# Performance work log

Hardware: AMD Instinct MI355X
Metric: run time of the kernel (lower is better)

The kernel has to match this reference:

```python
import jax, jax.numpy as jnp
import numpy as np

B, N, C, H = 2, 2048, 768, 12
D = C // H
EPS = 1e-5


def setup_inputs() -> dict:
    key = jax.random.key(0)
    ks = jax.random.split(key, 12)
    s = 0.02
    return {
        "x": jax.random.normal(ks[0], (B, N, C), jnp.float32),
        "attn_mask": jax.random.randint(ks[1], (N, N), 0, 2) > 0,  # True = NOT allowed
        "ln1_g": jnp.ones((C,), jnp.float32),
        "ln1_b": jnp.zeros((C,), jnp.float32),
        "w_qkv": jax.random.normal(ks[2], (C, 3 * C), jnp.float32) * s,  # [in,out]
        "b_qkv": jnp.zeros((3 * C,), jnp.float32),
        "w_proj": jax.random.normal(ks[3], (C, C), jnp.float32) * s,
        "b_proj": jnp.zeros((C,), jnp.float32),
        "ls1": jnp.full((C,), 1e-5, jnp.float32),
        "ln2_g": jnp.ones((C,), jnp.float32),
        "ln2_b": jnp.zeros((C,), jnp.float32),
        "w1": jax.random.normal(ks[4], (C, 4 * C), jnp.float32) * s,
        "b1": jnp.zeros((4 * C,), jnp.float32),
        "w2": jax.random.normal(ks[5], (4 * C, C), jnp.float32) * s,
        "b2": jnp.zeros((C,), jnp.float32),
        "ls2": jnp.full((C,), 1e-5, jnp.float32),
    }


def layer_norm(x, g, b):
    mu = jnp.mean(x, axis=-1, keepdims=True)
    var = jnp.var(x, axis=-1, keepdims=True)
    return (x - mu) * jax.lax.rsqrt(var + EPS) * g + b


def reference(x, attn_mask, ln1_g, ln1_b, w_qkv, b_qkv, w_proj, b_proj, ls1,
              ln2_g, ln2_b, w1, b1, w2, b2, ls2):
    # ---- attention branch ----
    h = layer_norm(x, ln1_g, ln1_b)
    qkv = h @ w_qkv + b_qkv                       # [B,N,3C]
    qkv = qkv.reshape(B, N, 3, H, D).transpose(2, 0, 3, 1, 4)  # [3,B,H,N,D]
    q, k, v = qkv[0], qkv[1], qkv[2]
    scores = jnp.einsum('bhnd,bhmd->bhnm', q, k) * (D ** -0.5)  # [B,H,N,N]
    neg = jnp.finfo(scores.dtype).min
    scores = jnp.where(attn_mask, neg, scores)    # mask broadcasts over B,H
    attn = jax.nn.softmax(scores, axis=-1)
    o = jnp.einsum('bhnm,bhmd->bhnd', attn, v).transpose(0, 2, 1, 3).reshape(B, N, C)
    x = x + (o @ w_proj + b_proj) * ls1
    # ---- MLP branch ----
    h = layer_norm(x, ln2_g, ln2_b)
    h = jax.nn.gelu(h @ w1 + b1, approximate=False)
    x = x + (h @ w2 + b2) * ls2
    return x
```

## Files before the change

### kernel.cpp

```cpp
#include <hip/hip_runtime.h>
#include <hip/hip_bf16.h>
#include <math.h>

#define BN 2
#define SEQ 2048
#define CH 768
#define NH 12
#define HD 64
#define TOK (BN*SEQ)


using bf16_t = __hip_bfloat16;
typedef __attribute__((ext_vector_type(8))) short short8;
typedef __attribute__((ext_vector_type(8))) unsigned short ushort8;
typedef __attribute__((ext_vector_type(4))) float floatx4;
typedef __attribute__((ext_vector_type(2))) unsigned uintx2;

#define OFF_LN1G 0
#define OFF_LN1B 768
#define OFF_BQKV 1536
#define OFF_BPROJ 3840
#define OFF_LS1 4608
#define OFF_LN2G 5376
#define OFF_LN2B 6144
#define OFF_B1 6912
#define OFF_B2 9984
#define OFF_LS2 10752

__device__ inline float b2f(bf16_t v){ return __bfloat162float(v); }
__device__ inline bf16_t f2b(float v){ return __float2bfloat16(v); }
__device__ inline short f2bs(float v){ bf16_t b = __float2bfloat16(v); return *reinterpret_cast<short*>(&b); }
__device__ inline unsigned pk2(float a, float b){
  return (unsigned)(unsigned short)f2bs(a) | ((unsigned)(unsigned short)f2bs(b) << 16);
}
__device__ inline float sane(float v){ return (fabsf(v) < 1e30f) ? v : 0.0f; }
__device__ inline float clampf(float v, float lim){
  v = sane(v);
  return fminf(fmaxf(v, -lim), lim);
}
__device__ inline float ldf(const bf16_t* p){ return __bfloat162float(*p); }
__device__ inline float ldf(const float* p){ return *p; }
__device__ inline bool bf16_mode(const void* gref){
  return *reinterpret_cast<const unsigned*>(gref) == 0x3F803F80u;
}
__device__ inline void gload16(const void* g, void* l){
  __builtin_amdgcn_global_load_lds(
      (const __attribute__((address_space(1))) unsigned int*)g,
      (__attribute__((address_space(3))) unsigned int*)l, 16, 0, 0);
}

template<typename T>
__device__ inline void tr32(const T* __restrict__ src, size_t colOff, int stride,
    bf16_t* __restrict__ dst, int dstStride, int r0, int c0, float* smem, int tid)
{
  const int tx = tid & 31, ty = tid >> 5;
  #pragma unroll
  for (int j = 0; j < 4; j++)
    smem[(ty + j*8)*33 + tx] = ldf(src + (size_t)(r0 + ty + j*8) * stride + colOff + c0 + tx);
  __syncthreads();
  #pragma unroll
  for (int j = 0; j < 4; j++)
    dst[(size_t)(c0 + ty + j*8) * dstStride + r0 + tx] = f2b(smem[tx*33 + ty + j*8]);
}

template<typename T, bool GUARDED>
__global__ __launch_bounds__(256) void prep1_kernel(
    const T* __restrict__ x, const T* __restrict__ w_qkv, const T* __restrict__ w_proj,
    const T* __restrict__ w1, const T* __restrict__ w2,
    const T* __restrict__ g1, const T* __restrict__ b1_, const T* __restrict__ bqkv,
    const T* __restrict__ bproj, const T* __restrict__ ls1, const T* __restrict__ g2,
    const T* __restrict__ b2_, const T* __restrict__ bb1, const T* __restrict__ bb2,
    const T* __restrict__ ls2, const void* __restrict__ mask,
    float* __restrict__ pb, bf16_t* __restrict__ wqkvT, bf16_t* __restrict__ wprojT,
    unsigned long long* __restrict__ m1, bf16_t* __restrict__ a1,
    bf16_t* __restrict__ w1T, bf16_t* __restrict__ w2T,
    const void* __restrict__ gref)
{
  if (GUARDED && (bf16_mode(gref) != (sizeof(T) == 2))) return;
  __shared__ float smem[1056];
  const int tid = threadIdx.x;
  int wg = blockIdx.x;

  if (wg < 4096) {
    const T* xr = x + (size_t)wg * CH;
    float v0 = sane(ldf(xr + tid)), v1 = sane(ldf(xr + tid + 256)), v2 = sane(ldf(xr + tid + 512));
    float s  = v0 + v1 + v2;
    float s2 = v0*v0 + v1*v1 + v2*v2;
    #pragma unroll
    for (int o = 32; o > 0; o >>= 1) { s += __shfl_down(s, o, 64); s2 += __shfl_down(s2, o, 64); }
    if ((tid & 63) == 0) { smem[tid >> 6] = s; smem[(tid >> 6) + 4] = s2; }
    __syncthreads();
    if (tid == 0) {
      float ts = smem[0] + smem[1] + smem[2] + smem[3];
      float tq = smem[4] + smem[5] + smem[6] + smem[7];
      float mu = ts * (1.f / CH);
      float var = tq * (1.f / CH) - mu * mu;
      smem[8] = mu; smem[9] = rsqrtf(fmaxf(var, 0.f) + 1e-5f);
    }
    __syncthreads();
    const float mu = smem[8], rs = smem[9];
    bf16_t* orow = a1 + (size_t)wg * CH;
    orow[tid      ] = f2b(clampf((v0 - mu) * rs * ldf(g1 + tid      ) + ldf(b1_ + tid      ), 32.f));
    orow[tid + 256] = f2b(clampf((v1 - mu) * rs * ldf(g1 + tid + 256) + ldf(b1_ + tid + 256), 32.f));
    orow[tid + 512] = f2b(clampf((v2 - mu) * rs * ldf(g1 + tid + 512) + ldf(b1_ + tid + 512), 32.f));
    return;
  }
  wg -= 4096;
  if (wg < 1728) {
    tr32(w_qkv, 0, 2304, wqkvT, 768, (wg / 72) * 32, (wg % 72) * 32, smem, tid);
    return;
  }
  wg -= 1728;
  if (wg < 576) {
    tr32(w_proj, 0, 768, wprojT, 768, (wg / 24) * 32, (wg % 24) * 32, smem, tid);
    return;
  }
  wg -= 576;
  if (wg < 512) {
    const unsigned* mw = (const unsigned*)mask;
    unsigned accu = 0;
    #pragma unroll 8
    for (int i = 0; i < 64; i++) accu |= mw[i];
    const bool is8 = (accu > 1u);
    const int wave = tid >> 6, lane = tid & 63;
    #pragma unroll 4
    for (int i = 0; i < 32; i++) {
      const int word = wg * 128 + wave * 32 + i;
      const size_t elem = (size_t)word * 64 + lane;
      bool pred;
      if (is8) pred = ((const unsigned char*)mask)[elem] != 0;
      else     pred = ((const int*)mask)[elem] != 0;
      unsigned long long bits = __ballot(pred);
      if (lane == 0) m1[word] = bits;
    }
    return;
  }
  wg -= 512;
  if (wg < 1) {
    #define PCOPY(off, src, n) for (int i = tid; i < (n); i += 256) pb[(off)+i] = ldf((src)+i);
    PCOPY(OFF_LN1G, g1, 768)
    PCOPY(OFF_LN1B, b1_, 768)
    PCOPY(OFF_BQKV, bqkv, 2304)
    PCOPY(OFF_BPROJ, bproj, 768)
    PCOPY(OFF_LS1, ls1, 768)
    PCOPY(OFF_LN2G, g2, 768)
    PCOPY(OFF_LN2B, b2_, 768)
    PCOPY(OFF_B1, bb1, 3072)
    PCOPY(OFF_B2, bb2, 768)
    PCOPY(OFF_LS2, ls2, 768)
    #undef PCOPY
    return;
  }
  wg -= 1;
  if (wg < 2304) {
    tr32(w1, 0, 3072, w1T, 768, (wg / 96) * 32, (wg % 96) * 32, smem, tid);
    return;
  }
  wg -= 2304;
  {
    tr32(w2, 0, 768, w2T, 3072, (wg / 24) * 32, (wg % 24) * 32, smem, tid);
    return;
  }
}

template<typename T, bool GUARDED>
__global__ __launch_bounds__(256) void trc_kernel(const T* __restrict__ w1,
    const T* __restrict__ w2, bf16_t* __restrict__ w1Tc, bf16_t* __restrict__ w2Tc,
    int kc, const void* __restrict__ gref)
{
  if (GUARDED && (bf16_mode(gref) != (sizeof(T) == 2))) return;
  __shared__ float smem[1056];
  const int tid = threadIdx.x;
  int wg = blockIdx.x;
  if (wg < 576) {
    tr32(w1, (size_t)kc * 768, 3072, w1Tc, 768, (wg / 24) * 32, (wg % 24) * 32, smem, tid);
  } else {
    wg -= 576;
    tr32(w2 + (size_t)kc * 768 * 768, 0, 768, w2Tc, 768, (wg / 24) * 32, (wg % 24) * 32, smem, tid);
  }
}

__global__ __launch_bounds__(256) void ln2x_kernel(const bf16_t* __restrict__ x1,
    bf16_t* __restrict__ a2, const float* __restrict__ pb)
{
  __shared__ float red[10];
  const int row = blockIdx.x, tid = threadIdx.x;
  const bf16_t* xr = x1 + (size_t)row * CH;
  float v0 = sane(ldf(xr + tid)), v1 = sane(ldf(xr + tid + 256)), v2 = sane(ldf(xr + tid + 512));
  float s  = v0 + v1 + v2;
  float s2 = v0*v0 + v1*v1 + v2*v2;
  #pragma unroll
  for (int o = 32; o > 0; o >>= 1) { s += __shfl_down(s, o, 64); s2 += __shfl_down(s2, o, 64); }
  if ((tid & 63) == 0) { red[tid >> 6] = s; red[(tid >> 6) + 4] = s2; }
  __syncthreads();
  if (tid == 0) {
    float ts = red[0] + red[1] + red[2] + red[3];
    float tq = red[4] + red[5] + red[6] + red[7];
    float mu = ts * (1.f / CH);
    float var = tq * (1.f / CH) - mu * mu;
    red[8] = mu; red[9] = rsqrtf(fmaxf(var, 0.f) + 1e-5f);
  }
  __syncthreads();
  const float mu = red[8], rs = red[9];
  bf16_t* orow = a2 + (size_t)row * CH;
  orow[tid      ] = f2b(clampf((v0 - mu) * rs * pb[OFF_LN2G + tid      ] + pb[OFF_LN2B + tid      ], 32.f));
  orow[tid + 256] = f2b(clampf((v1 - mu) * rs * pb[OFF_LN2G + tid + 256] + pb[OFF_LN2B + tid + 256], 32.f));
  orow[tid + 512] = f2b(clampf((v2 - mu) * rs * pb[OFF_LN2G + tid + 512] + pb[OFF_LN2B + tid + 512], 32.f));
}

template<int MODE, int MT, int NT>
__global__ __launch_bounds__(256) void mgemm(
    const bf16_t* __restrict__ A, const bf16_t* __restrict__ BT,
    const float* __restrict__ pb, const int K, const int ldb,
    const int biasOff, const int scaleOff,
    const void* __restrict__ resid, const void* __restrict__ gref,
    bf16_t* __restrict__ o0, bf16_t* __restrict__ o1, bf16_t* __restrict__ vtout,
    float* __restrict__ oF, const bf16_t* __restrict__ stg,
    const int addPrev, const int finalize)
{
  constexpr int MI = MT / 32;
  constexpr int NI = NT / 32;
  __shared__ __align__(16) short As[MT * 32];
  __shared__ __align__(16) short Bs[NT * 32];
  const int tid = threadIdx.x;
  const int wave = tid >> 6, lane = tid & 63, lane15 = lane & 15, quad = lane >> 4;
  const int wr = (wave >> 1) * (MT / 2), wc = (wave & 1) * (NT / 2);
  const int mBase = blockIdx.y * MT;
  const int nBase = blockIdx.x * NT;

  floatx4 acc[MI][NI];
  #pragma unroll
  for (int mi = 0; mi < MI; mi++)
    #pragma unroll
    for (int ni = 0; ni < NI; ni++) acc[mi][ni] = (floatx4){0.f, 0.f, 0.f, 0.f};

  const bf16_t* aS0 = A  + (size_t)(mBase + (tid >> 2)) * K + (tid & 3) * 8;
  const bf16_t* aS1 = aS0 + (size_t)64 * K;
  const bf16_t* bS0 = BT + (size_t)(nBase + (tid >> 2)) * ldb + (tid & 3) * 8;
  const bf16_t* bS1 = bS0 + (size_t)64 * ldb;
  const int wfl = __builtin_amdgcn_readfirstlane(wave);
  short* aD0 = &As[wfl * 512];
  short* aD1 = (MT == 128) ? &As[2048 + wfl * 512] : nullptr;
  short* bD0 = &Bs[wfl * 512];
  short* bD1 = (NT == 128) ? &Bs[2048 + wfl * 512] : nullptr;

  for (int k0 = 0; k0 < K; k0 += 32) {
    __syncthreads();
    gload16(aS0 + k0, aD0);
    if (MT == 128) gload16(aS1 + k0, aD1);
    gload16(bS0 + k0, bD0);
    if (NT == 128) gload16(bS1 + k0, bD1);
    __syncthreads();
    short8 av[MI], bv[NI];
    #pragma unroll
    for (int mi = 0; mi < MI; mi++)
      av[mi] = *(const short8*)&As[(wr + mi * 16 + lane15) * 32 + quad * 8];
    #pragma unroll
    for (int ni = 0; ni < NI; ni++)
      bv[ni] = *(const short8*)&Bs[(wc + ni * 16 + lane15) * 32 + quad * 8];
    #pragma unroll
    for (int mi = 0; mi < MI; mi++)
      #pragma unroll
      for (int ni = 0; ni < NI; ni++)
        acc[mi][ni] = __builtin_amdgcn_mfma_f32_16x16x32_bf16(av[mi], bv[ni], acc[mi][ni], 0, 0, 0);
  }

  const bool rbf = (MODE == 1) ? bf16_mode(gref) : false;
  #pragma unroll
  for (int mi = 0; mi < MI; mi++) {
    #pragma unroll
    for (int ni = 0; ni < NI; ni++) {
      const int c0u = nBase + wc + ni * 16;
      const int col = c0u + lane15;
      float bia = 0.f, sc = 0.f;
      if (MODE == 0 || MODE == 1 || MODE == 2) bia = pb[biasOff + col];
      if (MODE == 1) sc = pb[scaleOff + col];
      if (MODE == 3 && finalize) { bia = pb[biasOff + col]; sc = pb[scaleOff + col]; }
      if (MODE == 0 && c0u >= 2 * CH) {
        const int cv = col - 2 * CH;
        const int bh = (mBase >> 11) * NH + (cv >> 6);
        const int d = cv & 63;
        const int tok0 = (mBase + wr + mi * 16 + quad * 4) & (SEQ - 1);
        float tv[4];
        #pragma unroll
        for (int r = 0; r < 4; r++) tv[r] = clampf(acc[mi][ni][r] + bia, 20.f);
        uintx2 pk = (uintx2){ pk2(tv[0], tv[1]), pk2(tv[2], tv[3]) };
        *(uintx2*)(vtout + ((size_t)(bh * 64 + d)) * SEQ + tok0) = pk;
        continue;
      }
      #pragma unroll
      for (int r = 0; r < 4; r++) {
        const int row = mBase + wr + mi * 16 + quad * 4 + r;
        float v = acc[mi][ni][r];
        if (MODE == 0) {
          const bf16_t qv = f2b(clampf(v + bia, 20.f));
          if (col < CH) o0[(size_t)row * CH + col] = qv;
          else          o1[(size_t)row * CH + (col - CH)] = qv;
        } else if (MODE == 1) {
          const size_t ix = (size_t)row * CH + col;
          const float rx = rbf ? b2f(((const bf16_t*)resid)[ix]) : ((const float*)resid)[ix];
          const bf16_t xv = f2b(rx + clampf(sc * (v + bia), 0.5f));
          o0[ix] = xv;
          o1[ix] = xv;
        } else if (MODE == 2) {
          const float h = v + bia;
          const float g = 0.5f * h * (1.f + erff(h * 0.70710678118f));
          o0[(size_t)row * CH + col] = f2b(clampf(g, 50.f));
        } else {
          const size_t ix = (size_t)row * CH + col;
          if (addPrev) v += oF[ix];
          if (!finalize) oF[ix] = v;
          else oF[ix] = b2f(stg[ix]) + clampf(sc * (v + bia), 0.5f);
        }
      }
    }
  }
}

__global__ __launch_bounds__(256) void attn4_kernel(bf16_t* __restrict__ q,
    const bf16_t* __restrict__ kbuf, const bf16_t* __restrict__ vtb,
    const unsigned long long* __restrict__ m1)
{
  __shared__ __align__(16) short Ks[64 * 72];
  __shared__ __align__(16) short Vs[64 * 72];
  __shared__ unsigned Plds[4][32 * 17];
  const int bh = blockIdx.y, b = bh / NH, h = bh % NH;
  const int q0 = blockIdx.x * 64;
  const int tid = threadIdx.x;
  const int wave = tid >> 6, l15 = tid & 15, quad = (tid & 63) >> 4;
  const int srow = tid >> 2, scc = (tid & 3) * 16;
  const size_t kgbase = (size_t)(b * SEQ) * CH + h * HD;
  const size_t vgbase = (size_t)(bh * HD) * SEQ;
  const int qrow = q0 + wave * 16 + l15;

  short8 qf[2];
  {
    const unsigned short* qp = (const unsigned short*)q
        + (size_t)(b * SEQ + qrow) * CH + h * HD + quad * 8;
    qf[0] = *(const short8*)(qp);
    qf[1] = *(const short8*)(qp + 32);
  }
  const unsigned long long* mrow = m1 + (size_t)qrow * (SEQ / 64);

  float mreg = -1.1e4f, lreg = 0.f;
  floatx4 oacc[4] = {{0,0,0,0},{0,0,0,0},{0,0,0,0},{0,0,0,0}};
  unsigned* pw = &Plds[wave][0];

  const unsigned short* kp0 = (const unsigned short*)kbuf + kgbase + (size_t)srow * CH + scc;
  const unsigned short* vp0 = (const unsigned short*)vtb + vgbase + (size_t)srow * SEQ + scc;
  ushort8 kr0 = *(const ushort8*)(kp0);
  ushort8 kr1 = *(const ushort8*)(kp0 + 8);
  ushort8 vr0 = *(const ushort8*)(vp0);
  ushort8 vr1 = *(const ushort8*)(vp0 + 8);

  for (int k0 = 0; k0 < SEQ; k0 += 64) {
    __syncthreads();
    *(ushort8*)&Ks[srow * 72 + scc]     = kr0;
    *(ushort8*)&Ks[srow * 72 + scc + 8] = kr1;
    *(ushort8*)&Vs[srow * 72 + scc]     = vr0;
    *(ushort8*)&Vs[srow * 72 + scc + 8] = vr1;
    if (k0 + 64 < SEQ) {
      const unsigned short* kp = kp0 + (size_t)(k0 + 64) * CH;
      const unsigned short* vp = vp0 + (k0 + 64);
      kr0 = *(const ushort8*)(kp);
      kr1 = *(const ushort8*)(kp + 8);
      vr0 = *(const ushort8*)(vp);
      vr1 = *(const ushort8*)(vp + 8);
    }
    __syncthreads();

    const unsigned long long mw = mrow[k0 >> 6];
    float sv[4][4];
    float tmax = -1.0e30f;
    #pragma unroll
    for (int kb = 0; kb < 4; kb++) {
      floatx4 t = {0,0,0,0};
      short8 kf0 = *(const short8*)&Ks[(kb * 16 + l15) * 72 + quad * 8];
      short8 kf1 = *(const short8*)&Ks[(kb * 16 + l15) * 72 + 32 + quad * 8];
      t = __builtin_amdgcn_mfma_f32_16x16x32_bf16(kf0, qf[0], t, 0, 0, 0);
      t = __builtin_amdgcn_mfma_f32_16x16x32_bf16(kf1, qf[1], t, 0, 0, 0);
      #pragma unroll
      for (int r = 0; r < 4; r++) {
        float v = clampf(t[r] * 0.125f, 1e4f);
        if ((mw >> (kb * 16 + quad * 4 + r)) & 1ull) v = -1.0e30f;
        sv[kb][r] = v;
        tmax = fmaxf(tmax, v);
      }
    }
    tmax = fmaxf(tmax, __shfl_xor(tmax, 16, 64));
    tmax = fmaxf(tmax, __shfl_xor(tmax, 32, 64));

    if (__any(tmax > mreg)) {
      const float mnew = fmaxf(mreg, tmax);
      float alpha = __expf(mreg - mnew);
      alpha = (alpha <= 1.f) ? alpha : 0.f;
      lreg *= alpha;
      #pragma unroll
      for (int db = 0; db < 4; db++)
        #pragma unroll
        for (int r = 0; r < 4; r++) oacc[db][r] *= alpha;
      mreg = mnew;
    }

    float ls = 0.f;
    #pragma unroll
    for (int kb = 0; kb < 4; kb++) {
      float pr[4];
      #pragma unroll
      for (int r = 0; r < 4; r++) {
        const float pv = __expf(sv[kb][r] - mreg);
        pr[r] = pv;
        ls += pv;
      }
      pw[(8 * kb + 2 * quad)     * 17 + l15] = pk2(pr[0], pr[1]);
      pw[(8 * kb + 2 * quad + 1) * 17 + l15] = pk2(pr[2], pr[3]);
    }
    ls += __shfl_xor(ls, 16, 64);
    ls += __shfl_xor(ls, 32, 64);
    lreg += ls;

    #pragma unroll
    for (int s = 0; s < 2; s++) {
      union { unsigned u[4]; short8 s8; } pu;
      #pragma unroll
      for (int w = 0; w < 4; w++)
        pu.u[w] = pw[(16 * s + 4 * quad + w) * 17 + l15];
      #pragma unroll
      for (int db = 0; db < 4; db++) {
        short8 vf = *(const short8*)&Vs[(db * 16 + l15) * 72 + s * 32 + quad * 8];
        oacc[db] = __builtin_amdgcn_mfma_f32_16x16x32_bf16(vf, pu.s8, oacc[db], 0, 0, 0);
      }
    }
  }

  const float inv = 1.f / fmaxf(lreg, 1e-20f);
  unsigned short* op = (unsigned short*)q
      + (size_t)(b * SEQ + qrow) * CH + h * HD + quad * 4;
  #pragma unroll
  for (int db = 0; db < 4; db++) {
    const unsigned lo = pk2(clampf(oacc[db][0] * inv, 10.f), clampf(oacc[db][1] * inv, 10.f));
    const unsigned hi = pk2(clampf(oacc[db][2] * inv, 10.f), clampf(oacc[db][3] * inv, 10.f));
    *(uintx2*)(op + db * 16) = (uintx2){lo, hi};
  }
}

extern "C" void kernel_launch(void* const* d_in, const int* in_sizes, int n_in,
                              void* d_out, int out_size, void* d_ws, size_t ws_size,
                              hipStream_t stream) {
  const void* x      = d_in[0];
  const void* mask   = d_in[1];
  const void* ln1_g  = d_in[2];
  const void* ln1_b  = d_in[3];
  const void* w_qkv  = d_in[4];
  const void* b_qkv  = d_in[5];
  const void* w_proj = d_in[6];
  const void* b_proj = d_in[7];
  const void* ls1    = d_in[8];
  const void* ln2_g  = d_in[9];
  const void* ln2_b  = d_in[10];
  const void* w1     = d_in[11];
  const void* b1     = d_in[12];
  const void* w2     = d_in[13];
  const void* b2     = d_in[14];
  const void* ls2    = d_in[15];
  const void* gref   = ln1_g;

  char* ws = (char*)d_ws;
  float*  pb     = (float*)ws;
  bf16_t* a12    = (bf16_t*)(ws + 65536);
  bf16_t* vt     = (bf16_t*)(ws + 65536 + 6291456);
  bf16_t* stage  = vt;
  char*   r3     = ws + 65536 + 2 * 6291456;
  bf16_t* wqkvT  = (bf16_t*)r3;
  bf16_t* wprojT = (bf16_t*)(r3 + 3538944);
  bf16_t* hact   = (bf16_t*)r3;
  char*   r4     = ws + 65536 + 3 * 6291456;
  unsigned long long* mi1 = (unsigned long long*)r4;
  bf16_t* w1Tc   = (bf16_t*)r4;
  bf16_t* w2Tc   = (bf16_t*)(r4 + 1179648);
  char*   r5     = ws + 21299200;
  bf16_t* w1T    = (bf16_t*)r5;
  bf16_t* w2T    = (bf16_t*)(r5 + 4718592);
  bf16_t* dQ     = (bf16_t*)d_out;
  bf16_t* dK     = dQ + 3145728;
  float*  outF   = (float*)d_out;

  const long long xs = in_sizes ? (long long)in_sizes[0] : 0;
  const int mode = (xs == 6291456LL) ? 1 : (xs == 12582912LL ? 2 : 0);
  const bool doFull = (ws_size >= 30736384ULL);
  const int prepGrid = doFull ? 11521 : 6913;

  #define PREP_ARGS(T) (const T*)x, (const T*)w_qkv, (const T*)w_proj, (const T*)w1, (const T*)w2, \
      (const T*)ln1_g, (const T*)ln1_b, (const T*)b_qkv, (const T*)b_proj, (const T*)ls1, \
      (const T*)ln2_g, (const T*)ln2_b, (const T*)b1, (const T*)b2, (const T*)ls2, \
      mask, pb, wqkvT, wprojT, mi1, a12, w1T, w2T, gref
  if (mode == 1)      prep1_kernel<bf16_t, false><<<prepGrid, 256, 0, stream>>>(PREP_ARGS(bf16_t));
  else if (mode == 2) prep1_kernel<float,  false><<<prepGrid, 256, 0, stream>>>(PREP_ARGS(float));
  else {
    prep1_kernel<bf16_t, true><<<prepGrid, 256, 0, stream>>>(PREP_ARGS(bf16_t));
    prep1_kernel<float,  true><<<prepGrid, 256, 0, stream>>>(PREP_ARGS(float));
  }
  #undef PREP_ARGS

  mgemm<0, 128, 128><<<dim3(18, 32), 256, 0, stream>>>(a12, wqkvT, pb, 768, 768, OFF_BQKV, 0,
      nullptr, gref, dQ, dK, vt, nullptr, nullptr, 0, 0);
  attn4_kernel<<<dim3(SEQ / 64, BN * NH), 256, 0, stream>>>(dQ, dK, vt, mi1);
  mgemm<1, 64, 64><<<dim3(12, 64), 256, 0, stream>>>(dQ, wprojT, pb, 768, 768, OFF_BPROJ, OFF_LS1,
      x, gref, dK, stage, nullptr, nullptr, nullptr, 0, 0);
  ln2x_kernel<<<TOK, 256, 0, stream>>>(dK, a12, pb);
  for (int kc = 0; kc < 4; kc++) {
    const bf16_t* bt1; const bf16_t* bt2; int ldb2;
    if (doFull) {
      bt1 = w1T + (size_t)kc * 768 * 768;
      bt2 = w2T + (size_t)kc * 768;
      ldb2 = 3072;
    } else {
      if (mode == 1)      trc_kernel<bf16_t, false><<<1152, 256, 0, stream>>>((const bf16_t*)w1, (const bf16_t*)w2, w1Tc, w2Tc, kc, gref);
      else if (mode == 2) trc_kernel<float,  false><<<1152, 256, 0, stream>>>((const float*)w1,  (const float*)w2,  w1Tc, w2Tc, kc, gref);
      else {
        trc_kernel<bf16_t, true><<<1152, 256, 0, stream>>>((const bf16_t*)w1, (const bf16_t*)w2, w1Tc, w2Tc, kc, gref);
        trc_kernel<float,  true><<<1152, 256, 0, stream>>>((const float*)w1,  (const float*)w2,  w1Tc, w2Tc, kc, gref);
      }
      bt1 = w1Tc; bt2 = w2Tc; ldb2 = 768;
    }
    mgemm<2, 64, 64><<<dim3(12, 64), 256, 0, stream>>>(a12, bt1, pb, 768, 768, OFF_B1 + kc * 768, 0,
        nullptr, gref, hact, nullptr, nullptr, nullptr, nullptr, 0, 0);
    mgemm<3, 64, 64><<<dim3(12, 64), 256, 0, stream>>>(hact, bt2, pb, 768, ldb2, OFF_B2, OFF_LS2,
        nullptr, gref, nullptr, nullptr, nullptr, outF, stage, kc > 0 ? 1 : 0, kc == 3 ? 1 : 0);
  }
}
```

Baseline: 432.5 us.

## Double-buffer GEMM LDS tiles and raise MFMA priority in attention

The GEMM main loop now uses two LDS buffers. Global-to-LDS loads for the next K step are issued before the current step's MFMAs, with explicit vmcnt waits and raw s_barrier instead of two __syncthreads per step. This is meant to overlap memory latency with compute, at the cost of doubling LDS per block, which may reduce occupancy. The attention kernel wraps its MFMA groups in s_setprio and drops the clamp on scaled scores, which removes a little ALU work but also a safety bound on the scores.

```diff
diff --git a/kernel.cpp b/kernel.cpp
--- a/kernel.cpp
+++ b/kernel.cpp
@@ -220,8 +220,9 @@
 {
   constexpr int MI = MT / 32;
   constexpr int NI = NT / 32;
-  __shared__ __align__(16) short As[MT * 32];
-  __shared__ __align__(16) short Bs[NT * 32];
+  constexpr int LOADS = MT / 64 + NT / 64;
+  __shared__ __align__(16) short As[2][MT * 32];
+  __shared__ __align__(16) short Bs[2][NT * 32];
   const int tid = threadIdx.x;
   const int wave = tid >> 6, lane = tid & 63, lane15 = lane & 15, quad = lane >> 4;
   const int wr = (wave >> 1) * (MT / 2), wc = (wave & 1) * (NT / 2);
@@ -239,30 +240,45 @@
   const bf16_t* bS0 = BT + (size_t)(nBase + (tid >> 2)) * ldb + (tid & 3) * 8;
   const bf16_t* bS1 = bS0 + (size_t)64 * ldb;
   const int wfl = __builtin_amdgcn_readfirstlane(wave);
-  short* aD0 = &As[wfl * 512];
-  short* aD1 = (MT == 128) ? &As[2048 + wfl * 512] : nullptr;
-  short* bD0 = &Bs[wfl * 512];
-  short* bD1 = (NT == 128) ? &Bs[2048 + wfl * 512] : nullptr;
-
-  for (int k0 = 0; k0 < K; k0 += 32) {
-    __syncthreads();
-    gload16(aS0 + k0, aD0);
-    if (MT == 128) gload16(aS1 + k0, aD1);
-    gload16(bS0 + k0, bD0);
-    if (NT == 128) gload16(bS1 + k0, bD1);
-    __syncthreads();
+  short* aD0 = &As[0][wfl * 512];
+  short* aD1 = (MT == 128) ? &As[0][2048 + wfl * 512] : nullptr;
+  short* bD0 = &Bs[0][wfl * 512];
+  short* bD1 = (NT == 128) ? &Bs[0][2048 + wfl * 512] : nullptr;
+
+  auto STAGE = [&](int buf, int k0) {
+    const int ab = buf * (MT * 32), bb = buf * (NT * 32);
+    gload16(aS0 + k0, aD0 + ab);
+    if (MT == 128) gload16(aS1 + k0, aD1 + ab);
+    gload16(bS0 + k0, bD0 + bb);
+    if (NT == 128) gload16(bS1 + k0, bD1 + bb);
+  };
+
+  const int nsteps = K / 32;
+  STAGE(0, 0);
+  for (int t = 0; t < nsteps; ++t) {
+    const int cur = t & 1;
+    if (t + 1 < nsteps) {
+      STAGE(cur ^ 1, (t + 1) * 32);
+      if constexpr (LOADS == 2)      asm volatile("s_waitcnt vmcnt(2)" ::: "memory");
+      else if constexpr (LOADS == 3) asm volatile("s_waitcnt vmcnt(3)" ::: "memory");
+      else                           asm volatile("s_waitcnt vmcnt(4)" ::: "memory");
+    } else {
+      asm volatile("s_waitcnt vmcnt(0)" ::: "memory");
+    }
+    __builtin_amdgcn_s_barrier();
     short8 av[MI], bv[NI];
     #pragma unroll
     for (int mi = 0; mi < MI; mi++)
-      av[mi] = *(const short8*)&As[(wr + mi * 16 + lane15) * 32 + quad * 8];
+      av[mi] = *(const short8*)&As[cur][(wr + mi * 16 + lane15) * 32 + quad * 8];
     #pragma unroll
     for (int ni = 0; ni < NI; ni++)
-      bv[ni] = *(const short8*)&Bs[(wc + ni * 16 + lane15) * 32 + quad * 8];
+      bv[ni] = *(const short8*)&Bs[cur][(wc + ni * 16 + lane15) * 32 + quad * 8];
     #pragma unroll
     for (int mi = 0; mi < MI; mi++)
       #pragma unroll
       for (int ni = 0; ni < NI; ni++)
         acc[mi][ni] = __builtin_amdgcn_mfma_f32_16x16x32_bf16(av[mi], bv[ni], acc[mi][ni], 0, 0, 0);
+    __builtin_amdgcn_s_barrier();
   }
 
   const bool rbf = (MODE == 1) ? bf16_mode(gref) : false;
@@ -317,7 +333,7 @@
   }
 }
 
-__global__ __launch_bounds__(256) void attn4_kernel(bf16_t* __restrict__ q,
+__global__ __launch_bounds__(256) void attn5_kernel(bf16_t* __restrict__ q,
     const bf16_t* __restrict__ kbuf, const bf16_t* __restrict__ vtb,
     const unsigned long long* __restrict__ m1)
 {
@@ -377,11 +393,13 @@
       floatx4 t = {0,0,0,0};
       short8 kf0 = *(const short8*)&Ks[(kb * 16 + l15) * 72 + quad * 8];
       short8 kf1 = *(const short8*)&Ks[(kb * 16 + l15) * 72 + 32 + quad * 8];
+      __builtin_amdgcn_s_setprio(1);
       t = __builtin_amdgcn_mfma_f32_16x16x32_bf16(kf0, qf[0], t, 0, 0, 0);
       t = __builtin_amdgcn_mfma_f32_16x16x32_bf16(kf1, qf[1], t, 0, 0, 0);
+      __builtin_amdgcn_s_setprio(0);
       #pragma unroll
       for (int r = 0; r < 4; r++) {
-        float v = clampf(t[r] * 0.125f, 1e4f);
+        float v = t[r] * 0.125f;
         if ((mw >> (kb * 16 + quad * 4 + r)) & 1ull) v = -1.0e30f;
         sv[kb][r] = v;
         tmax = fmaxf(tmax, v);
@@ -425,11 +443,13 @@
       #pragma unroll
       for (int w = 0; w < 4; w++)
         pu.u[w] = pw[(16 * s + 4 * quad + w) * 17 + l15];
+      __builtin_amdgcn_s_setprio(1);
       #pragma unroll
       for (int db = 0; db < 4; db++) {
         short8 vf = *(const short8*)&Vs[(db * 16 + l15) * 72 + s * 32 + quad * 8];
         oacc[db] = __builtin_amdgcn_mfma_f32_16x16x32_bf16(vf, pu.s8, oacc[db], 0, 0, 0);
       }
+      __builtin_amdgcn_s_setprio(0);
     }
   }
 
@@ -504,7 +524,7 @@
 
   mgemm<0, 128, 128><<<dim3(18, 32), 256, 0, stream>>>(a12, wqkvT, pb, 768, 768, OFF_BQKV, 0,
       nullptr, gref, dQ, dK, vt, nullptr, nullptr, 0, 0);
-  attn4_kernel<<<dim3(SEQ / 64, BN * NH), 256, 0, stream>>>(dQ, dK, vt, mi1);
+  attn5_kernel<<<dim3(SEQ / 64, BN * NH), 256, 0, stream>>>(dQ, dK, vt, mi1);
   mgemm<1, 64, 64><<<dim3(12, 64), 256, 0, stream>>>(dQ, wprojT, pb, 768, 768, OFF_BPROJ, OFF_LS1,
       x, gref, dK, stage, nullptr, nullptr, nullptr, 0, 0);
   ln2x_kernel<<<TOK, 256, 0, stream>>>(dK, a12, pb);
```

New measurement: 420.3 us. 1.03x faster.
